# Performance work log

Hardware: AMD Instinct MI355X
Metric: run time of the kernel (lower is better)

The kernel has to match this reference:

```python
import jax, jax.numpy as jnp
import numpy as np

EPS = 1e-5
SLOPE = 0.2


def _gather(points, idx):
    # points: [B, N, C], idx: [B, S] -> [B, S, C]
    return jnp.take_along_axis(points, idx[..., None], axis=1)


def _block(x, W, b, g, be):
    # Linear -> BatchNorm1d (training-mode batch stats over (B, S)) -> LeakyReLU(0.2)
    y = jnp.einsum("bsc,dc->bsd", x, W) + b
    mu = jnp.mean(y, axis=(0, 1))
    var = jnp.mean((y - mu) ** 2, axis=(0, 1))  # biased var, as torch BN uses for normalization
    y = (y - mu) * jax.lax.rsqrt(var + EPS) * g + be
    return jnp.where(y >= 0, y, SLOPE * y)


def setup_inputs() -> dict:
    c0, c1, c2, c3, c4 = 64, 128, 256, 512, 1024
    B = 64
    N0, N1, N2, N3, N4 = 2048, 1024, 512, 256, 128
    keys = iter(jax.random.split(jax.random.key(0), 40))
    inp = {"num_point": 128}
    inp["f0"] = jax.random.normal(next(keys), (B, N0, c0), jnp.float32)
    inp["f1"] = jax.random.normal(next(keys), (B, N1, c1), jnp.float32)
    inp["f2"] = jax.random.normal(next(keys), (B, N2, c2), jnp.float32)
    inp["f3"] = jax.random.normal(next(keys), (B, N3, c3), jnp.float32)
    inp["f4"] = jax.random.normal(next(keys), (B, N4, c4), jnp.float32)
    inp["FPS_0"] = jax.random.randint(next(keys), (B, N1), 0, N0)
    inp["FPS_1"] = jax.random.randint(next(keys), (B, N2), 0, N1)
    inp["FPS_2"] = jax.random.randint(next(keys), (B, N3), 0, N2)
    inp["FPS_3"] = jax.random.randint(next(keys), (B, N4), 0, N3)
    for name, cin, cout in [("04", c0, c4), ("14", c1, c4), ("24", c2, c4), ("34", c3, c4), ("4", c4, c4)]:
        inp[f"w{name}"] = jax.random.normal(next(keys), (cout, cin), jnp.float32) / np.sqrt(cin).astype(np.float32)
        inp[f"b{name}"] = jax.random.normal(next(keys), (cout,), jnp.float32) * 0.01
        inp[f"g{name}"] = jnp.ones((cout,), jnp.float32)
        inp[f"be{name}"] = jnp.zeros((cout,), jnp.float32)
    return inp


def reference(num_point, f0, f1, f2, f3, f4, FPS_0, FPS_1, FPS_2, FPS_3,
              w04, b04, g04, be04, w14, b14, g14, be14,
              w24, b24, g24, be24, w34, b34, g34, be34,
              w4, b4, g4, be4):
    # num_point == 128 branch: nested index chains down to the coarsest resolution
    idx24 = jnp.take_along_axis(FPS_2, FPS_3, axis=1)   # [B, 128] indices into N2
    idx14 = jnp.take_along_axis(FPS_1, idx24, axis=1)   # [B, 128] indices into N1
    idx04 = jnp.take_along_axis(FPS_0, idx14, axis=1)   # [B, 128] indices into N0
    f04 = _block(_gather(f0, idx04), w04, b04, g04, be04)
    f14 = _block(_gather(f1, idx14), w14, b14, g14, be14)
    f24 = _block(_gather(f2, idx24), w24, b24, g24, be24)
    f34 = _block(_gather(f3, FPS_3), w34, b34, g34, be34)
    f4_new = _block(f4 + f04 + f14 + f24 + f34, w4, b4, g4, be4) + f4
    return (f0, f1, f2, f3, f4_new)
```

## Files before the change

kernel.cpp:

```cpp
#include <hip/hip_runtime.h>
#include <hip/hip_bf16.h>
#include <type_traits>

using bf16 = __hip_bfloat16;
typedef __attribute__((ext_vector_type(8))) short short8;
typedef __attribute__((ext_vector_type(4))) float floatx4;

struct alignas(16) bf16x8 { bf16 v[8]; };

#define EPSV 1e-5f

__device__ __forceinline__ float lrelu(float v) { return v >= 0.f ? v : 0.2f * v; }

__device__ __forceinline__ uint4 f8_to_bf8(const float* __restrict__ p) {
    float4 a = ((const float4*)p)[0];
    float4 b = ((const float4*)p)[1];
    bf16x8 r;
    r.v[0] = __float2bfloat16(a.x); r.v[1] = __float2bfloat16(a.y);
    r.v[2] = __float2bfloat16(a.z); r.v[3] = __float2bfloat16(a.w);
    r.v[4] = __float2bfloat16(b.x); r.v[5] = __float2bfloat16(b.y);
    r.v[6] = __float2bfloat16(b.z); r.v[7] = __float2bfloat16(b.w);
    return *(uint4*)&r;
}

__global__ __launch_bounds__(256) void copy4_k(
    const float* __restrict__ f0, const float* __restrict__ f1,
    const float* __restrict__ f2, const float* __restrict__ f3,
    float* __restrict__ out)
{
    int region = blockIdx.y;
    const float* src = (region == 0) ? f0 : (region == 1) ? f1 : (region == 2) ? f2 : f3;
    size_t off = ((size_t)blockIdx.x * 256 + threadIdx.x) * 8;
    float* dst = out + (size_t)region * 8388608 + off;
    ((uint4*)dst)[0] = ((const uint4*)(src + off))[0];
    ((uint4*)dst)[1] = ((const uint4*)(src + off))[1];
}

__global__ void idx_k(const int* __restrict__ FPS0, const int* __restrict__ FPS1,
                      const int* __restrict__ FPS2, const int* __restrict__ FPS3,
                      int* __restrict__ rowidx)
{
    int b = blockIdx.x;
    int s = threadIdx.x;
    int i3 = FPS3[b * 128 + s];
    int i2 = FPS2[b * 256 + i3];
    int i1 = FPS1[b * 512 + i2];
    int i0 = FPS0[b * 1024 + i1];
    int m = b * 128 + s;
    rowidx[0 * 8192 + m] = b * 2048 + i0;
    rowidx[1 * 8192 + m] = b * 1024 + i1;
    rowidx[2 * 8192 + m] = b * 512 + i2;
    rowidx[3 * 8192 + m] = b * 256 + i3;
    rowidx[4 * 8192 + m] = m;
}

template <typename AT>
__global__ __launch_bounds__(256) void gemm_bt(
    const AT* __restrict__ A, const float* __restrict__ W,
    bf16* __restrict__ Y, const int* __restrict__ rowidx, int K,
    float* __restrict__ sums)
{
    __shared__ bf16 As[128][40];
    __shared__ bf16 Bs[128][40];

    int tid = threadIdx.x;
    int bm = blockIdx.x, bn = blockIdx.y;

    int r0 = tid >> 2;
    int r1 = r0 + 64;
    int c0 = (tid & 3) << 3;
    const AT* a0 = A + (size_t)rowidx[bm * 128 + r0] * K + c0;
    const AT* a1 = A + (size_t)rowidx[bm * 128 + r1] * K + c0;
    const float* b0 = W + (size_t)(bn * 128 + r0) * K + c0;
    const float* b1 = W + (size_t)(bn * 128 + r1) * K + c0;

    int lane = tid & 63, wave = tid >> 6;
    int wm = (wave >> 1) << 6;
    int wn = (wave & 1) << 6;
    int lm = lane & 15;
    int kq = (lane >> 4) << 3;

    floatx4 acc[4][4] = {};

    for (int k0 = 0; k0 < K; k0 += 32) {
        if constexpr (std::is_same<AT, float>::value) {
            *(uint4*)&As[r0][c0] = f8_to_bf8(a0 + k0);
            *(uint4*)&As[r1][c0] = f8_to_bf8(a1 + k0);
        } else {
            *(uint4*)&As[r0][c0] = *(const uint4*)(a0 + k0);
            *(uint4*)&As[r1][c0] = *(const uint4*)(a1 + k0);
        }
        *(uint4*)&Bs[r0][c0] = f8_to_bf8(b0 + k0);
        *(uint4*)&Bs[r1][c0] = f8_to_bf8(b1 + k0);
        __syncthreads();

        short8 af[4], bfr[4];
#pragma unroll
        for (int i = 0; i < 4; i++) af[i]  = *(const short8*)&As[wm + i * 16 + lm][kq];
#pragma unroll
        for (int j = 0; j < 4; j++) bfr[j] = *(const short8*)&Bs[wn + j * 16 + lm][kq];
#pragma unroll
        for (int i = 0; i < 4; i++)
#pragma unroll
            for (int j = 0; j < 4; j++)
                acc[i][j] = __builtin_amdgcn_mfma_f32_16x16x32_bf16(af[i], bfr[j], acc[i][j], 0, 0, 0);
        __syncthreads();
    }

    int mrow = (lane >> 4) << 2;
    int ncol = lane & 15;
    float ps[4] = {}, pq[4] = {};
#pragma unroll
    for (int i = 0; i < 4; i++) {
#pragma unroll
        for (int j = 0; j < 4; j++) {
#pragma unroll
            for (int r = 0; r < 4; r++) {
                int m = (bm << 7) + wm + i * 16 + mrow + r;
                int n = (bn << 7) + wn + j * 16 + ncol;
                bf16 bv = __float2bfloat16(acc[i][j][r]);
                Y[(size_t)m * 1024 + n] = bv;
                float v = __bfloat162float(bv);
                ps[j] += v; pq[j] += v * v;
            }
        }
    }
#pragma unroll
    for (int j = 0; j < 4; j++) {
        ps[j] += __shfl_xor(ps[j], 16); ps[j] += __shfl_xor(ps[j], 32);
        pq[j] += __shfl_xor(pq[j], 16); pq[j] += __shfl_xor(pq[j], 32);
    }
    if (lane < 16) {
#pragma unroll
        for (int j = 0; j < 4; j++) {
            int ch = (bn << 7) + wn + (j << 4) + lane;
            atomicAdd(&sums[ch], ps[j]);
            atomicAdd(&sums[1024 + ch], pq[j]);
        }
    }
}

__global__ void finalize_k(const float* __restrict__ sums, float* __restrict__ ss,
                           const float* g0, const float* be0, const float* g1, const float* be1,
                           const float* g2, const float* be2, const float* g3, const float* be3,
                           const float* g4, const float* be4, int slot0)
{
    int slot = slot0 + blockIdx.y;
    int ch = blockIdx.x * 256 + threadIdx.x;
    const float *g, *be;
    switch (slot) {
        case 0: g = g0; be = be0; break;
        case 1: g = g1; be = be1; break;
        case 2: g = g2; be = be2; break;
        case 3: g = g3; be = be3; break;
        default: g = g4; be = be4; break;
    }
    float sum = sums[slot * 2048 + ch];
    float sq  = sums[slot * 2048 + 1024 + ch];
    float mu  = sum * (1.f / 8192.f);
    float var = sq * (1.f / 8192.f) - mu * mu;
    float sc  = g[ch] * rsqrtf(var + EPSV);
    float sh  = be[ch] - mu * sc;
    ss[slot * 2048 + ch] = sc;
    ss[slot * 2048 + 1024 + ch] = sh;
}

__global__ __launch_bounds__(256) void combine_k(
    const bf16* __restrict__ Y0, const bf16* __restrict__ Y1,
    const bf16* __restrict__ Y2, const bf16* __restrict__ Y3,
    const float* __restrict__ f4, const float* __restrict__ ss,
    bf16* __restrict__ X4)
{
    size_t base = ((size_t)blockIdx.x * 256 + threadIdx.x) * 8;
    int cq = (int)((base & 1023) >> 2);
    const floatx4* ssv = (const floatx4*)ss;
    floatx4 sc[4][2], sh[4][2];
#pragma unroll
    for (int br = 0; br < 4; br++) {
        sc[br][0] = ssv[br * 512 + cq];
        sc[br][1] = ssv[br * 512 + cq + 1];
        sh[br][0] = ssv[br * 512 + 256 + cq];
        sh[br][1] = ssv[br * 512 + 256 + cq + 1];
    }
    bf16x8 y0 = *(const bf16x8*)(Y0 + base);
    bf16x8 y1 = *(const bf16x8*)(Y1 + base);
    bf16x8 y2 = *(const bf16x8*)(Y2 + base);
    bf16x8 y3 = *(const bf16x8*)(Y3 + base);
    float4 v4a = ((const float4*)(f4 + base))[0];
    float4 v4b = ((const float4*)(f4 + base))[1];
    float v4[8] = {v4a.x, v4a.y, v4a.z, v4a.w, v4b.x, v4b.y, v4b.z, v4b.w};
    bf16x8 o;
#pragma unroll
    for (int k = 0; k < 8; k++) {
        int h = k >> 2, l = k & 3;
        float x = v4[k];
        x += lrelu(__bfloat162float(y0.v[k]) * sc[0][h][l] + sh[0][h][l]);
        x += lrelu(__bfloat162float(y1.v[k]) * sc[1][h][l] + sh[1][h][l]);
        x += lrelu(__bfloat162float(y2.v[k]) * sc[2][h][l] + sh[2][h][l]);
        x += lrelu(__bfloat162float(y3.v[k]) * sc[3][h][l] + sh[3][h][l]);
        o.v[k] = __float2bfloat16(x);
    }
    *(bf16x8*)(X4 + base) = o;
}

__global__ __launch_bounds__(256) void final_k(
    const bf16* __restrict__ Y4, const float* __restrict__ f4,
    const float* __restrict__ ss4, float* __restrict__ out4)
{
    size_t base = ((size_t)blockIdx.x * 256 + threadIdx.x) * 8;
    int cq = (int)((base & 1023) >> 2);
    const floatx4* ssv = (const floatx4*)ss4;
    floatx4 sc0 = ssv[cq], sc1 = ssv[cq + 1];
    floatx4 sh0 = ssv[256 + cq], sh1 = ssv[256 + cq + 1];
    bf16x8 y  = *(const bf16x8*)(Y4 + base);
    float4 v4a = ((const float4*)(f4 + base))[0];
    float4 v4b = ((const float4*)(f4 + base))[1];
    float v4[8] = {v4a.x, v4a.y, v4a.z, v4a.w, v4b.x, v4b.y, v4b.z, v4b.w};
    float o[8];
#pragma unroll
    for (int k = 0; k < 8; k++) {
        float sc = (k < 4) ? sc0[k & 3] : sc1[k & 3];
        float sh = (k < 4) ? sh0[k & 3] : sh1[k & 3];
        float v = __bfloat162float(y.v[k]) * sc + sh;
        o[k] = lrelu(v) + v4[k];
    }
    ((float4*)(out4 + base))[0] = make_float4(o[0], o[1], o[2], o[3]);
    ((float4*)(out4 + base))[1] = make_float4(o[4], o[5], o[6], o[7]);
}

extern "C" void kernel_launch(void* const* d_in, const int* in_sizes, int n_in,
                              void* d_out, int out_size, void* d_ws, size_t ws_size,
                              hipStream_t stream)
{
    const float* f0 = (const float*)d_in[1];
    const float* f1 = (const float*)d_in[2];
    const float* f2 = (const float*)d_in[3];
    const float* f3 = (const float*)d_in[4];
    const float* f4 = (const float*)d_in[5];
    const int* FPS0 = (const int*)d_in[6];
    const int* FPS1 = (const int*)d_in[7];
    const int* FPS2 = (const int*)d_in[8];
    const int* FPS3 = (const int*)d_in[9];
    const float* w04 = (const float*)d_in[10];
    const float* g04 = (const float*)d_in[12];
    const float* be04 = (const float*)d_in[13];
    const float* w14 = (const float*)d_in[14];
    const float* g14 = (const float*)d_in[16];
    const float* be14 = (const float*)d_in[17];
    const float* w24 = (const float*)d_in[18];
    const float* g24 = (const float*)d_in[20];
    const float* be24 = (const float*)d_in[21];
    const float* w34 = (const float*)d_in[22];
    const float* g34 = (const float*)d_in[24];
    const float* be34 = (const float*)d_in[25];
    const float* w4 = (const float*)d_in[26];
    const float* g4 = (const float*)d_in[28];
    const float* be4 = (const float*)d_in[29];

    float* out = (float*)d_out;

    const size_t YN = (size_t)8192 * 1024;
    bf16* Y0 = (bf16*)d_ws;
    bf16* Y1 = Y0 + YN;
    bf16* Y2 = Y1 + YN;
    bf16* Y3 = Y2 + YN;
    int* rowidx = (int*)(Y3 + YN);
    float* sums = (float*)(rowidx + 5 * 8192);
    float* ss = sums + 5 * 2048;
    bf16* X4 = Y0;
    bf16* Y4 = Y1;

    if (ws_size < (size_t)(4 * YN * 2 + 5 * 8192 * 4 + 2 * 5 * 2048 * 4)) return;

    hipMemsetAsync(sums, 0, 5 * 2048 * sizeof(float), stream);

    copy4_k<<<dim3(4096, 4), 256, 0, stream>>>(f0, f1, f2, f3, out);
    idx_k<<<64, 128, 0, stream>>>(FPS0, FPS1, FPS2, FPS3, rowidx);

    gemm_bt<float><<<dim3(64, 8), 256, 0, stream>>>(f0, w04, Y0, rowidx + 0 * 8192, 64,   sums + 0 * 2048);
    gemm_bt<float><<<dim3(64, 8), 256, 0, stream>>>(f1, w14, Y1, rowidx + 1 * 8192, 128,  sums + 1 * 2048);
    gemm_bt<float><<<dim3(64, 8), 256, 0, stream>>>(f2, w24, Y2, rowidx + 2 * 8192, 256,  sums + 2 * 2048);
    gemm_bt<float><<<dim3(64, 8), 256, 0, stream>>>(f3, w34, Y3, rowidx + 3 * 8192, 512,  sums + 3 * 2048);

    finalize_k<<<dim3(4, 4), 256, 0, stream>>>(sums, ss, g04, be04, g14, be14, g24, be24,
                                               g34, be34, g4, be4, 0);
    combine_k<<<4096, 256, 0, stream>>>(Y0, Y1, Y2, Y3, f4, ss, X4);

    gemm_bt<bf16><<<dim3(64, 8), 256, 0, stream>>>(X4, w4, Y4, rowidx + 4 * 8192, 1024, sums + 4 * 2048);

    finalize_k<<<dim3(4, 1), 256, 0, stream>>>(sums, ss, g04, be04, g14, be14, g24, be24,
                                               g34, be34, g4, be4, 4);
    final_k<<<4096, 256, 0, stream>>>(Y4, f4, ss + 4 * 2048, out + (size_t)4 * 8388608);
}
```

Measured before the change: 516.4 us.

## Pre-gather to bf16 and use async global-to-LDS loads in batched GEMM

Adds a gather kernel that converts the indexed rows of f0..f3 and all weights to bf16 in contiguous scratch, using the unused out4 region as storage. The GEMM then loads tiles straight into LDS with global_load_lds, with no register staging or conversion, and the four level GEMMs run as one launch over a z grid dimension. This aims to cut per-tile load and convert overhead and launch count, at the cost of an extra gather pass through memory. The LDS tiles lose their padding, so bank conflicts may appear.

```diff
diff --git a/kernel.cpp b/kernel.cpp
--- a/kernel.cpp
+++ b/kernel.cpp
@@ -1,6 +1,5 @@
 #include <hip/hip_runtime.h>
 #include <hip/hip_bf16.h>
-#include <type_traits>
 
 using bf16 = __hip_bfloat16;
 typedef __attribute__((ext_vector_type(8))) short short8;
@@ -21,6 +20,13 @@
     r.v[4] = __float2bfloat16(b.x); r.v[5] = __float2bfloat16(b.y);
     r.v[6] = __float2bfloat16(b.z); r.v[7] = __float2bfloat16(b.w);
     return *(uint4*)&r;
+}
+
+__device__ __forceinline__ void async16(void* lds, const void* g) {
+    __builtin_amdgcn_global_load_lds(
+        (const __attribute__((address_space(1))) void*)g,
+        (__attribute__((address_space(3))) void*)lds,
+        16, 0, 0);
 }
 
 __global__ __launch_bounds__(256) void copy4_k(
@@ -54,25 +60,69 @@
     rowidx[4 * 8192 + m] = m;
 }
 
-template <typename AT>
-__global__ __launch_bounds__(256) void gemm_bt(
-    const AT* __restrict__ A, const float* __restrict__ W,
-    bf16* __restrict__ Y, const int* __restrict__ rowidx, int K,
-    float* __restrict__ sums)
-{
-    __shared__ bf16 As[128][40];
-    __shared__ bf16 Bs[128][40];
+__global__ __launch_bounds__(256) void gather_k(
+    const float* __restrict__ f0, const float* __restrict__ f1,
+    const float* __restrict__ f2, const float* __restrict__ f3,
+    const float* __restrict__ w04, const float* __restrict__ w14,
+    const float* __restrict__ w24, const float* __restrict__ w34,
+    const float* __restrict__ w4,
+    const int* __restrict__ rowidx, bf16* __restrict__ Ab, bf16* __restrict__ Wb)
+{
+    int slot = blockIdx.y;
+    size_t e = ((size_t)blockIdx.x * 256 + threadIdx.x) * 8;
+    if (slot < 4) {
+        int L = slot;
+        int lk = 6 + L;
+        size_t total = (size_t)8192 << lk;
+        if (e >= total) return;
+        int K = 1 << lk;
+        int row = (int)(e >> lk);
+        int col = (int)(e & (size_t)(K - 1));
+        const float* src = (L == 0) ? f0 : (L == 1) ? f1 : (L == 2) ? f2 : f3;
+        int gr = rowidx[L * 8192 + row];
+        uint4 r = f8_to_bf8(src + (size_t)gr * K + col);
+        *(uint4*)(Ab + (size_t)8192 * ((64 << L) - 64) + e) = r;
+    } else {
+        int L = slot - 4;
+        int lk = 6 + L;
+        size_t total = (size_t)1024 << lk;
+        if (e >= total) return;
+        const float* src = (L == 0) ? w04 : (L == 1) ? w14 : (L == 2) ? w24
+                         : (L == 3) ? w34 : w4;
+        uint4 r = f8_to_bf8(src + e);
+        *(uint4*)(Wb + (size_t)1024 * ((64 << L) - 64) + e) = r;
+    }
+}
+
+__global__ __launch_bounds__(256) void gemm16_k(
+    const bf16* __restrict__ Ab, const bf16* __restrict__ Wb,
+    bf16* __restrict__ Ybase, float* __restrict__ sums, int level0)
+{
+    __shared__ bf16 As[128 * 32];
+    __shared__ bf16 Bs[128 * 32];
+
+    int z = blockIdx.z;
+    int L = level0 + z;
+    int K = 64 << L;
+    const bf16* A = Ab + (size_t)8192 * ((L < 4) ? ((64 << L) - 64) : 0);
+    const bf16* W = Wb + (size_t)1024 * ((64 << L) - 64);
+    bf16* Y = Ybase + (size_t)z * (8192 * 1024);
+    float* sm = sums + z * 2048;
 
     int tid = threadIdx.x;
     int bm = blockIdx.x, bn = blockIdx.y;
 
-    int r0 = tid >> 2;
-    int r1 = r0 + 64;
-    int c0 = (tid & 3) << 3;
-    const AT* a0 = A + (size_t)rowidx[bm * 128 + r0] * K + c0;
-    const AT* a1 = A + (size_t)rowidx[bm * 128 + r1] * K + c0;
-    const float* b0 = W + (size_t)(bn * 128 + r0) * K + c0;
-    const float* b1 = W + (size_t)(bn * 128 + r1) * K + c0;
+    int u0 = tid, u1 = tid + 256;
+    int row0 = u0 >> 2, k80 = (u0 & 3) << 3;
+    int row1 = u1 >> 2, k81 = (u1 & 3) << 3;
+    const bf16* ga0 = A + ((size_t)(bm * 128 + row0) * K + k80);
+    const bf16* ga1 = A + ((size_t)(bm * 128 + row1) * K + k81);
+    const bf16* gb0 = W + ((size_t)(bn * 128 + row0) * K + k80);
+    const bf16* gb1 = W + ((size_t)(bn * 128 + row1) * K + k81);
+    bf16* la0 = As + u0 * 8;
+    bf16* la1 = As + u1 * 8;
+    bf16* lb0 = Bs + u0 * 8;
+    bf16* lb1 = Bs + u1 * 8;
 
     int lane = tid & 63, wave = tid >> 6;
     int wm = (wave >> 1) << 6;
@@ -83,22 +133,18 @@
     floatx4 acc[4][4] = {};
 
     for (int k0 = 0; k0 < K; k0 += 32) {
-        if constexpr (std::is_same<AT, float>::value) {
-            *(uint4*)&As[r0][c0] = f8_to_bf8(a0 + k0);
-            *(uint4*)&As[r1][c0] = f8_to_bf8(a1 + k0);
-        } else {
-            *(uint4*)&As[r0][c0] = *(const uint4*)(a0 + k0);
-            *(uint4*)&As[r1][c0] = *(const uint4*)(a1 + k0);
-        }
-        *(uint4*)&Bs[r0][c0] = f8_to_bf8(b0 + k0);
-        *(uint4*)&Bs[r1][c0] = f8_to_bf8(b1 + k0);
+        async16(la0, ga0);
+        async16(la1, ga1);
+        async16(lb0, gb0);
+        async16(lb1, gb1);
+        ga0 += 32; ga1 += 32; gb0 += 32; gb1 += 32;
         __syncthreads();
 
         short8 af[4], bfr[4];
 #pragma unroll
-        for (int i = 0; i < 4; i++) af[i]  = *(const short8*)&As[wm + i * 16 + lm][kq];
-#pragma unroll
-        for (int j = 0; j < 4; j++) bfr[j] = *(const short8*)&Bs[wn + j * 16 + lm][kq];
+        for (int i = 0; i < 4; i++) af[i]  = *(const short8*)&As[(wm + i * 16 + lm) * 32 + kq];
+#pragma unroll
+        for (int j = 0; j < 4; j++) bfr[j] = *(const short8*)&Bs[(wn + j * 16 + lm) * 32 + kq];
 #pragma unroll
         for (int i = 0; i < 4; i++)
 #pragma unroll
@@ -134,8 +180,8 @@
 #pragma unroll
         for (int j = 0; j < 4; j++) {
             int ch = (bn << 7) + wn + (j << 4) + lane;
-            atomicAdd(&sums[ch], ps[j]);
-            atomicAdd(&sums[1024 + ch], pq[j]);
+            atomicAdd(&sm[ch], ps[j]);
+            atomicAdd(&sm[1024 + ch], pq[j]);
         }
     }
 }
@@ -270,25 +316,29 @@
     bf16* X4 = Y0;
     bf16* Y4 = Y1;
 
+    float* out4 = out + (size_t)4 * 8388608;
+    bf16* Ab = (bf16*)out4;
+    bf16* Wb = Ab + (size_t)8192 * 960;
+
     if (ws_size < (size_t)(4 * YN * 2 + 5 * 8192 * 4 + 2 * 5 * 2048 * 4)) return;
 
     hipMemsetAsync(sums, 0, 5 * 2048 * sizeof(float), stream);
 
+    idx_k<<<64, 128, 0, stream>>>(FPS0, FPS1, FPS2, FPS3, rowidx);
     copy4_k<<<dim3(4096, 4), 256, 0, stream>>>(f0, f1, f2, f3, out);
-    idx_k<<<64, 128, 0, stream>>>(FPS0, FPS1, FPS2, FPS3, rowidx);
-
-    gemm_bt<float><<<dim3(64, 8), 256, 0, stream>>>(f0, w04, Y0, rowidx + 0 * 8192, 64,   sums + 0 * 2048);
-    gemm_bt<float><<<dim3(64, 8), 256, 0, stream>>>(f1, w14, Y1, rowidx + 1 * 8192, 128,  sums + 1 * 2048);
-    gemm_bt<float><<<dim3(64, 8), 256, 0, stream>>>(f2, w24, Y2, rowidx + 2 * 8192, 256,  sums + 2 * 2048);
-    gemm_bt<float><<<dim3(64, 8), 256, 0, stream>>>(f3, w34, Y3, rowidx + 3 * 8192, 512,  sums + 3 * 2048);
+    gather_k<<<dim3(2048, 9), 256, 0, stream>>>(f0, f1, f2, f3,
+                                                w04, w14, w24, w34, w4,
+                                                rowidx, Ab, Wb);
+
+    gemm16_k<<<dim3(64, 8, 4), 256, 0, stream>>>(Ab, Wb, Y0, sums, 0);
 
     finalize_k<<<dim3(4, 4), 256, 0, stream>>>(sums, ss, g04, be04, g14, be14, g24, be24,
                                                g34, be34, g4, be4, 0);
     combine_k<<<4096, 256, 0, stream>>>(Y0, Y1, Y2, Y3, f4, ss, X4);
 
-    gemm_bt<bf16><<<dim3(64, 8), 256, 0, stream>>>(X4, w4, Y4, rowidx + 4 * 8192, 1024, sums + 4 * 2048);
+    gemm16_k<<<dim3(64, 8, 1), 256, 0, stream>>>(X4, Wb, Y4, sums + 4 * 2048, 4);
 
     finalize_k<<<dim3(4, 1), 256, 0, stream>>>(sums, ss, g04, be04, g14, be14, g24, be24,
                                                g34, be34, g4, be4, 4);
-    final_k<<<4096, 256, 0, stream>>>(Y4, f4, ss + 4 * 2048, out + (size_t)4 * 8388608);
-}
+    final_k<<<4096, 256, 0, stream>>>(Y4, f4, ss + 4 * 2048, out4);
+}
```

Result: faster. 467.1 us (-9.5%).
